# Kernel optimization log

Measured on AMD Instinct MI355X. Metric: run time of the kernel, lower is better.

The kernel has to match this reference:

```python
import jax, jax.numpy as jnp
import numpy as np

# Cost coefficients from MatcherConfig (init_kwargs)
C_CLASS, C_MASK, C_DICE, C_DIST, C_NLL, C_LIK = 2.0, 5.0, 5.0, 1.0, 0.5, 0.5

B, P, Q, E = 8, 16384, 256, 128  # images, pixels (H*W), queries, electrons


def setup_inputs() -> dict:
    key = jax.random.key(0)
    ks = jax.random.split(key, 8)
    mask_mask = jax.random.uniform(ks[0], (B, P, Q)) < 0.10           # sparsity pattern of pred logits
    mask_logit_values = jax.random.normal(ks[1], (B, P, Q), jnp.float32)
    seg_occ = jax.random.uniform(ks[2], (B, P, E)) < 0.05              # sparsity pattern of target segmap
    seg_vals = jax.random.uniform(ks[3], (B, P, E), jnp.float32, 1e-3, 1.0)
    segmap_values = jnp.where(seg_occ, seg_vals, 0.0)
    pred_logits = jax.random.normal(ks[4], (B, Q), jnp.float32)
    pred_positions = jax.random.uniform(ks[5], (B, Q, 2), jnp.float32)
    true_positions = jax.random.uniform(ks[6], (B, E, 2), jnp.float32)
    kd, ko = jax.random.split(ks[7])
    diag = 1.0 + 2.0 * jax.random.uniform(kd, (B, Q, 2), jnp.float32)  # positive diag of scale_tril
    off = 0.3 * jax.random.normal(ko, (B, Q), jnp.float32)
    pred_chol = jnp.zeros((B, Q, 2, 2), jnp.float32)
    pred_chol = pred_chol.at[..., 0, 0].set(diag[..., 0])
    pred_chol = pred_chol.at[..., 1, 1].set(diag[..., 1])
    pred_chol = pred_chol.at[..., 1, 0].set(off)
    image_sizes_xy = jnp.full((B, 2), 128.0, jnp.float32)
    return {
        'pred_logits': pred_logits,
        'mask_logit_values': mask_logit_values,
        'mask_mask': mask_mask,
        'segmap_values': segmap_values,
        'pred_positions': pred_positions,
        'pred_chol': pred_chol,
        'true_positions': true_positions,
        'image_sizes_xy': image_sizes_xy,
    }


def _total_cost(pred_logits, mask_logit_values, segmap_values, pred_positions,
                pred_chol, true_positions, image_sizes_xy, mask_mask):
    sp = jax.nn.softplus
    m = mask_mask
    # --- class cost: BCE(logit, 1) per query -> [B,Q]
    class_cost = sp(-pred_logits)
    # --- mask BCE cost (get_bce_cost): sparse entries only
    pos = jnp.where(m, sp(-mask_logit_values), 0.0)   # BCE vs 1 on nnz entries
    neg = jnp.where(m, sp(mask_logit_values), 0.0)    # BCE vs 0 on nnz entries
    targ = (segmap_values > 0).astype(pos.dtype)      # binarized target segmap
    pos_loss = jnp.einsum('bpq,bpe->bqe', pos, targ)
    neg_loss = neg.sum(1)[:, :, None] - jnp.einsum('bpq,bpe->bqe', neg, targ)
    nnz = jnp.maximum(targ.sum((1, 2)), 1.0)          # target _nnz() per image
    mask_cost = (pos_loss + neg_loss) / nnz[:, None, None]
    # --- dice cost (get_dice_cost): sparse softmax over query dim
    NEG = jnp.asarray(-1e30, mask_logit_values.dtype)
    z = jnp.where(m, mask_logit_values, NEG)
    mx = jnp.max(z, axis=-1, keepdims=True)
    ez = jnp.where(m, jnp.exp(z - mx), 0.0)
    s = ez.sum(-1, keepdims=True)
    pred_p = jnp.where(s > 0, ez / jnp.maximum(s, 1e-30), 0.0)  # [B,P,Q]
    num = 2.0 * jnp.einsum('bpq,bpe->bqe', pred_p, segmap_values)
    den = pred_p.sum(1)[:, :, None] + segmap_values.sum(1)[:, None, :]
    dice_cost = 1.0 - (num + 1.0) / (den + 1.0)
    # --- huber distance cost (delta=1), mean over xy
    d = pred_positions[:, :, None, :] - true_positions[:, None, :, :]  # [B,Q,E,2]
    ad = jnp.abs(d)
    huber_cost = jnp.where(ad < 1.0, 0.5 * d * d, ad - 0.5).mean(-1)
    # --- NLL / likelihood distance costs (MVN with scale_tril)
    mu = pred_positions * image_sizes_xy[:, None, :]
    y = true_positions * image_sizes_xy[:, None, :]
    diff = y[:, None, :, :] - mu[:, :, None, :]        # [B,Q,E,2]
    L00 = pred_chol[..., 0, 0][:, :, None]
    L10 = pred_chol[..., 1, 0][:, :, None]
    L11 = pred_chol[..., 1, 1][:, :, None]
    z0 = diff[..., 0] / L00
    z1 = (diff[..., 1] - L10 * z0) / L11
    nll_cost = 0.5 * (z0 * z0 + z1 * z1) + jnp.log(2.0 * jnp.pi) + jnp.log(L00) + jnp.log(L11)
    lik_cost = 1.0 - jnp.exp(-nll_cost)
    total = (C_CLASS * class_cost[:, :, None] + C_MASK * mask_cost + C_DICE * dice_cost
             + C_DIST * huber_cost + C_NLL * nll_cost + C_LIK * lik_cost)
    return total  # [B, Q, E] stacked per-image cost matrices


def reference(pred_logits, mask_logit_values, mask_mask, segmap_values,
              pred_positions, pred_chol, true_positions, image_sizes_xy):
    return _total_cost(pred_logits, mask_logit_values, segmap_values, pred_positions,
                       pred_chol, true_positions, image_sizes_xy, mask_mask)
```

## Files before the change

kernel.cpp:

```cpp
#include <hip/hip_runtime.h>
#include <cstdint>
#include <cstddef>

typedef float v4f __attribute__((ext_vector_type(4)));
typedef short short8 __attribute__((ext_vector_type(8)));
typedef unsigned short ushort_t;

constexpr int B_ = 8, P_ = 16384, Q_ = 256, E_ = 128;

__device__ __forceinline__ unsigned int f2bf(float f) {
  unsigned int x = __float_as_uint(f);
  x += 0x7FFFu + ((x >> 16) & 1u);
  return x >> 16;
}
__device__ __forceinline__ float softplus_f(float x) {
  return fmaxf(x, 0.f) + __logf(1.f + __expf(-fabsf(x)));
}
__device__ __forceinline__ void gload16(const void* g, void* l) {
  __builtin_amdgcn_global_load_lds((const __attribute__((address_space(1))) void*)g,
                                   (__attribute__((address_space(3))) void*)l,
                                   16, 0, 0);
}

__global__ __launch_bounds__(256, 4) void prep_rows(
    const float* __restrict__ mlv, const int* __restrict__ mask,
    ushort_t* __restrict__ A1T, ushort_t* __restrict__ PPT,
    float* __restrict__ negsum, float* __restrict__ ppsum)
{
  __shared__ unsigned int st[256 * 33];
  const int t = threadIdx.x, w = t >> 6, l = t & 63;
  const int b = blockIdx.x >> 8, cp = blockIdx.x & 255;
  const size_t base = ((size_t)b * P_ + cp * 64) * Q_;
  float accN[4] = {0.f,0.f,0.f,0.f}, accP[4] = {0.f,0.f,0.f,0.f};
  unsigned int a1w[4][4][2], ppw[4][4][2];

#pragma unroll
  for (int g = 0; g < 4; ++g) {
#pragma unroll
    for (int j = 0; j < 4; ++j) { a1w[g][j][0]=0; a1w[g][j][1]=0; ppw[g][j][0]=0; ppw[g][j][1]=0; }
#pragma unroll
    for (int r = 0; r < 4; ++r) {
      const int pl = (w << 4) + (g << 2) + r;
      const float* xp = mlv + base + (size_t)pl * Q_ + l;
      const int*   mp = mask + base + (size_t)pl * Q_ + l;
      float xs[4]; int ms[4];
#pragma unroll
      for (int j = 0; j < 4; ++j) { xs[j] = xp[j * 64]; ms[j] = mp[j * 64]; }
      float ev[4]; float s = 0.f;
#pragma unroll
      for (int j = 0; j < 4; ++j) {
        const bool mm = ms[j] != 0;
        const float xv = xs[j];
        const float e = mm ? __expf(xv) : 0.f;
        ev[j] = e; s += e;
        accN[j] += __logf(1.f + e);
        a1w[g][j][r >> 1] |= f2bf(mm ? -xv : 0.f) << ((r & 1) * 16);
      }
#pragma unroll
      for (int o = 32; o; o >>= 1) s += __shfl_xor(s, o, 64);
      const float inv = (s > 0.f) ? (1.f / s) : 0.f;
#pragma unroll
      for (int j = 0; j < 4; ++j) {
        const float p = ev[j] * inv;
        accP[j] += p;
        ppw[g][j][r >> 1] |= f2bf(p) << ((r & 1) * 16);
      }
    }
  }
  const size_t tb = ((size_t)(b * 256 + cp)) * 16384;
#pragma unroll
  for (int g = 0; g < 4; ++g)
#pragma unroll
    for (int j = 0; j < 4; ++j) {
      const int wb = (l + (j << 6)) * 33 + (w << 3) + (g << 1);
      st[wb] = a1w[g][j][0]; st[wb + 1] = a1w[g][j][1];
    }
  __syncthreads();
  {
    uint4* dst = (uint4*)(A1T + tb);
#pragma unroll
    for (int pass = 0; pass < 8; ++pass) {
      const int gi = pass * 256 + t;
      const int q = gi >> 3, c = (gi & 7) ^ (q & 7);
      const int wd = q * 33 + c * 4;
      uint4 v; v.x = st[wd]; v.y = st[wd+1]; v.z = st[wd+2]; v.w = st[wd+3];
      dst[gi] = v;
    }
  }
  __syncthreads();
#pragma unroll
  for (int g = 0; g < 4; ++g)
#pragma unroll
    for (int j = 0; j < 4; ++j) {
      const int wb = (l + (j << 6)) * 33 + (w << 3) + (g << 1);
      st[wb] = ppw[g][j][0]; st[wb + 1] = ppw[g][j][1];
    }
  __syncthreads();
  {
    uint4* dst = (uint4*)(PPT + tb);
#pragma unroll
    for (int pass = 0; pass < 8; ++pass) {
      const int gi = pass * 256 + t;
      const int q = gi >> 3, c = (gi & 7) ^ (q & 7);
      const int wd = q * 33 + c * 4;
      uint4 v; v.x = st[wd]; v.y = st[wd+1]; v.z = st[wd+2]; v.w = st[wd+3];
      dst[gi] = v;
    }
  }
  __syncthreads();
  float* red = (float*)st;
#pragma unroll
  for (int j = 0; j < 4; ++j) red[w * 256 + l + (j << 6)] = accN[j];
  __syncthreads();
  {
    const float sn = red[t] + red[256 + t] + red[512 + t] + red[768 + t];
    atomicAdd(&negsum[b * 256 + t], sn);
  }
  __syncthreads();
#pragma unroll
  for (int j = 0; j < 4; ++j) red[w * 256 + l + (j << 6)] = accP[j];
  __syncthreads();
  {
    const float sq = red[t] + red[256 + t] + red[512 + t] + red[768 + t];
    atomicAdd(&ppsum[b * 256 + t], sq);
  }
}

__global__ __launch_bounds__(256, 4) void prep_seg(
    const float* __restrict__ seg, ushort_t* __restrict__ SGT, ushort_t* __restrict__ SGB,
    float* __restrict__ segsum, float* __restrict__ nnzb)
{
  __shared__ unsigned int st[128 * 33];
  const int t = threadIdx.x, w = t >> 6, l = t & 63;
  const int b = blockIdx.x >> 8, cp = blockIdx.x & 255;
  const size_t base = ((size_t)b * P_ + cp * 64) * E_;
  float accS[2] = {0.f, 0.f}; float cnt = 0.f;
  unsigned int sgw[4][2][2], sbw[4][2][2];
#pragma unroll
  for (int g = 0; g < 4; ++g) {
#pragma unroll
    for (int j = 0; j < 2; ++j) { sgw[g][j][0]=0; sgw[g][j][1]=0; sbw[g][j][0]=0; sbw[g][j][1]=0; }
#pragma unroll
    for (int r = 0; r < 4; ++r) {
      const int pl = (w << 4) + (g << 2) + r;
      const float* vp = seg + base + (size_t)pl * E_ + l;
#pragma unroll
      for (int j = 0; j < 2; ++j) {
        const float v = vp[j * 64];
        const bool nz = v > 0.f;
        accS[j] += v; cnt += nz ? 1.f : 0.f;
        sgw[g][j][r >> 1] |= f2bf(v) << ((r & 1) * 16);
        sbw[g][j][r >> 1] |= (nz ? 0x3F80u : 0u) << ((r & 1) * 16);
      }
    }
  }
  const size_t tb = ((size_t)(b * 256 + cp)) * 8192;
#pragma unroll
  for (int g = 0; g < 4; ++g)
#pragma unroll
    for (int j = 0; j < 2; ++j) {
      const int wb = (l + (j << 6)) * 33 + (w << 3) + (g << 1);
      st[wb] = sgw[g][j][0]; st[wb + 1] = sgw[g][j][1];
    }
  __syncthreads();
  {
    uint4* dst = (uint4*)(SGT + tb);
#pragma unroll
    for (int pass = 0; pass < 4; ++pass) {
      const int gi = pass * 256 + t;
      const int q = gi >> 3, c = (gi & 7) ^ (q & 7);
      const int wd = q * 33 + c * 4;
      uint4 v; v.x = st[wd]; v.y = st[wd+1]; v.z = st[wd+2]; v.w = st[wd+3];
      dst[gi] = v;
    }
  }
  __syncthreads();
#pragma unroll
  for (int g = 0; g < 4; ++g)
#pragma unroll
    for (int j = 0; j < 2; ++j) {
      const int wb = (l + (j << 6)) * 33 + (w << 3) + (g << 1);
      st[wb] = sbw[g][j][0]; st[wb + 1] = sbw[g][j][1];
    }
  __syncthreads();
  {
    uint4* dst = (uint4*)(SGB + tb);
#pragma unroll
    for (int pass = 0; pass < 4; ++pass) {
      const int gi = pass * 256 + t;
      const int q = gi >> 3, c = (gi & 7) ^ (q & 7);
      const int wd = q * 33 + c * 4;
      uint4 v; v.x = st[wd]; v.y = st[wd+1]; v.z = st[wd+2]; v.w = st[wd+3];
      dst[gi] = v;
    }
  }
  __syncthreads();
  float* red = (float*)st;
#pragma unroll
  for (int j = 0; j < 2; ++j) red[w * 128 + l + (j << 6)] = accS[j];
  __syncthreads();
  if (t < 128) {
    const float ss = red[t] + red[128 + t] + red[256 + t] + red[384 + t];
    atomicAdd(&segsum[b * 128 + t], ss);
  }
#pragma unroll
  for (int o = 32; o; o >>= 1) cnt += __shfl_xor(cnt, o, 64);
  if (l == 0) atomicAdd(&nnzb[b], cnt);
}

__global__ __launch_bounds__(256, 2) void gemm_mfma(
    const ushort_t* __restrict__ A1T, const ushort_t* __restrict__ PPT,
    const ushort_t* __restrict__ SGT, const ushort_t* __restrict__ SGB,
    float* __restrict__ part)
{
  __shared__ __align__(16) char lds[32768];
  const int id = blockIdx.x;
  const int ks = id & 15, qt = (id >> 4) & 1, g = (id >> 5) & 1, b = id >> 6;
  const ushort_t* Aall = g ? PPT : A1T;
  const ushort_t* Ball = g ? SGT : SGB;
  const int t = threadIdx.x, l = t & 63, w = t >> 6;
  const int lm = l & 15, quad = l >> 4;
  const int wm = w & 1, wn = w >> 1;
  v4f acc[4][4];
#pragma unroll
  for (int i = 0; i < 4; ++i)
#pragma unroll
    for (int j = 0; j < 4; ++j) acc[i][j] = (v4f)0.f;
  const size_t cp0 = (size_t)b * 256 + ks * 16;
  const char* gA = (const char*)(Aall + cp0 * 16384 + qt * 8192);
  const char* gB = (const char*)(Ball + cp0 * 8192);
  const int off = t * 16;

  for (int it = 0; it < 16; ++it) {
    __syncthreads();
    const char* pa = gA + (size_t)it * 32768;
    const char* pb = gB + (size_t)it * 16384;
    gload16(pa + off,          lds + off);
    gload16(pa + off + 4096,   lds + off + 4096);
    gload16(pa + off + 8192,   lds + off + 8192);
    gload16(pa + off + 12288,  lds + off + 12288);
    gload16(pb + off,          lds + 16384 + off);
    gload16(pb + off + 4096,   lds + 16384 + off + 4096);
    gload16(pb + off + 8192,   lds + 16384 + off + 8192);
    gload16(pb + off + 12288,  lds + 16384 + off + 12288);
    __syncthreads();
#pragma unroll
    for (int k32 = 0; k32 < 2; ++k32) {
      short8 af[4], bf[4];
      const int ach = ((k32 << 2) | quad) ^ (lm & 7);
#pragma unroll
      for (int i = 0; i < 4; ++i) {
        af[i] = *(const short8*)(lds + (wm * 64 + i * 16 + lm) * 128 + ach * 16);
        bf[i] = *(const short8*)(lds + 16384 + (wn * 64 + i * 16 + lm) * 128 + ach * 16);
      }
#pragma unroll
      for (int i = 0; i < 4; ++i)
#pragma unroll
        for (int j = 0; j < 4; ++j)
          acc[i][j] = __builtin_amdgcn_mfma_f32_16x16x32_bf16(af[i], bf[j], acc[i][j], 0, 0, 0);
    }
  }
  float* pout = part + (size_t)(g * 8 + b) * 32768;
#pragma unroll
  for (int i = 0; i < 4; ++i)
#pragma unroll
    for (int r = 0; r < 4; ++r) {
      const int q = qt * 128 + wm * 64 + i * 16 + quad * 4 + r;
#pragma unroll
      for (int j = 0; j < 4; ++j) {
        const int e = wn * 64 + j * 16 + lm;
        atomicAdd(&pout[q * 128 + e], acc[i][j][r]);
      }
    }
}

__global__ __launch_bounds__(128) void epilogue(
    const float* __restrict__ part,
    const float* __restrict__ negsum, const float* __restrict__ ppsum,
    const float* __restrict__ segsum, const float* __restrict__ nnzb,
    const float* __restrict__ logits, const float* __restrict__ ppos,
    const float* __restrict__ chol, const float* __restrict__ tpos,
    const float* __restrict__ imgsz, float* __restrict__ out)
{
  const int bq = blockIdx.x;
  const int b = bq >> 8;
  const int e = threadIdx.x;
  const int qe = (bq & 255) * 128 + e;
  const float g1 = part[(size_t)b * 32768 + qe];
  const float g2 = part[(size_t)(8 + b) * 32768 + qe];

  const float nnz = fmaxf(nnzb[b], 1.f);
  const float mask_cost = (negsum[bq] + g1) / nnz;
  const float dice = 1.f - (2.f * g2 + 1.f) / (ppsum[bq] + segsum[b * 128 + e] + 1.f);
  const float cls = softplus_f(-logits[bq]);
  const float px = ppos[bq * 2], py = ppos[bq * 2 + 1];
  const float tx = tpos[(b * 128 + e) * 2], ty = tpos[(b * 128 + e) * 2 + 1];
  const float dx = px - tx, dy = py - ty;
  const float ax = fabsf(dx), ay = fabsf(dy);
  const float hx = (ax < 1.f) ? 0.5f * dx * dx : ax - 0.5f;
  const float hy = (ay < 1.f) ? 0.5f * dy * dy : ay - 0.5f;
  const float huber = 0.5f * (hx + hy);
  const float sx = imgsz[b * 2], sy = imgsz[b * 2 + 1];
  const float L00 = chol[bq * 4 + 0], L10 = chol[bq * 4 + 2], L11 = chol[bq * 4 + 3];
  const float d0 = (tx - px) * sx, d1 = (ty - py) * sy;
  const float z0 = d0 / L00;
  const float z1 = (d1 - L10 * z0) / L11;
  const float nll = 0.5f * (z0 * z0 + z1 * z1) + 1.8378770664093453f + __logf(L00) + __logf(L11);
  const float lik = 1.f - __expf(-nll);
  out[bq * 128 + e] = 2.f * cls + 5.f * mask_cost + 5.f * dice + huber + 0.5f * nll + 0.5f * lik;
}

extern "C" void kernel_launch(void* const* d_in, const int* in_sizes, int n_in,
                              void* d_out, int out_size, void* d_ws, size_t ws_size,
                              hipStream_t stream)
{
  (void)in_sizes; (void)n_in; (void)out_size; (void)ws_size;
  const float* logits = (const float*)d_in[0];
  const float* mlv    = (const float*)d_in[1];
  const int*   mask   = (const int*)d_in[2];
  const float* seg    = (const float*)d_in[3];
  const float* ppos   = (const float*)d_in[4];
  const float* chol   = (const float*)d_in[5];
  const float* tpos   = (const float*)d_in[6];
  const float* imgsz  = (const float*)d_in[7];

  char* ws = (char*)d_ws;
  ushort_t* A1T = (ushort_t*)(ws);
  ushort_t* PPT = (ushort_t*)(ws + 67108864);
  ushort_t* SGT = (ushort_t*)(ws + 134217728);
  ushort_t* SGB = (ushort_t*)(ws + 167772160);
  float* part   = (float*)(ws + 201326592);
  float* negsum = (float*)(ws + 203423744);
  float* ppsum  = (float*)(ws + 203431936);
  float* segsum = (float*)(ws + 203440128);
  float* nnzb   = (float*)(ws + 203444224);

  hipMemsetAsync(ws + 201326592, 0, 2117696, stream);
  prep_seg<<<2048, 256, 0, stream>>>(seg, SGT, SGB, segsum, nnzb);
  prep_rows<<<2048, 256, 0, stream>>>(mlv, mask, A1T, PPT, negsum, ppsum);
  gemm_mfma<<<512, 256, 0, stream>>>(A1T, PPT, SGT, SGB, part);
  epilogue<<<2048, 128, 0, stream>>>(part, negsum, ppsum, segsum, nnzb,
                                     logits, ppos, chol, tpos, imgsz, (float*)d_out);
}
```

Before: 512.6 us.

## Vectorize prep kernel loads with float4, prefetching, and a new LDS transpose layout

Both preprocessing kernels now have each lane read four consecutive columns with 16-byte loads and prefetch the next row pair. They pack bf16 pairs of adjacent rows in registers and write them to LDS in a row-major padded layout, then read it back transposed. prep_seg builds the binary mask tile from the bf16 value tile during the store, so it needs one LDS staging pass instead of two. The goal is fewer, wider global load instructions and less LDS traffic in these memory-bound kernels. The cost is more register pressure and strided LDS reads, which may cause bank conflicts.

Result: slower. 523.4 us (+2.1%).

```diff
diff --git a/kernel.cpp b/kernel.cpp
--- a/kernel.cpp
+++ b/kernel.cpp
@@ -27,181 +27,168 @@
     ushort_t* __restrict__ A1T, ushort_t* __restrict__ PPT,
     float* __restrict__ negsum, float* __restrict__ ppsum)
 {
-  __shared__ unsigned int st[256 * 33];
+  __shared__ unsigned int st[32 * 260];
   const int t = threadIdx.x, w = t >> 6, l = t & 63;
   const int b = blockIdx.x >> 8, cp = blockIdx.x & 255;
-  const size_t base = ((size_t)b * P_ + cp * 64) * Q_;
+  const size_t base = ((size_t)b * P_ + (size_t)cp * 64) * Q_;
+  const float* rbase = mlv + base + (size_t)(w * 16) * Q_ + 4 * l;
+  const int*   mbase = mask + base + (size_t)(w * 16) * Q_ + 4 * l;
   float accN[4] = {0.f,0.f,0.f,0.f}, accP[4] = {0.f,0.f,0.f,0.f};
-  unsigned int a1w[4][4][2], ppw[4][4][2];
-
-#pragma unroll
-  for (int g = 0; g < 4; ++g) {
-#pragma unroll
-    for (int j = 0; j < 4; ++j) { a1w[g][j][0]=0; a1w[g][j][1]=0; ppw[g][j][0]=0; ppw[g][j][1]=0; }
-#pragma unroll
-    for (int r = 0; r < 4; ++r) {
-      const int pl = (w << 4) + (g << 2) + r;
-      const float* xp = mlv + base + (size_t)pl * Q_ + l;
-      const int*   mp = mask + base + (size_t)pl * Q_ + l;
-      float xs[4]; int ms[4];
-#pragma unroll
-      for (int j = 0; j < 4; ++j) { xs[j] = xp[j * 64]; ms[j] = mp[j * 64]; }
-      float ev[4]; float s = 0.f;
-#pragma unroll
-      for (int j = 0; j < 4; ++j) {
-        const bool mm = ms[j] != 0;
-        const float xv = xs[j];
-        const float e = mm ? __expf(xv) : 0.f;
-        ev[j] = e; s += e;
-        accN[j] += __logf(1.f + e);
-        a1w[g][j][r >> 1] |= f2bf(mm ? -xv : 0.f) << ((r & 1) * 16);
-      }
-#pragma unroll
-      for (int o = 32; o; o >>= 1) s += __shfl_xor(s, o, 64);
-      const float inv = (s > 0.f) ? (1.f / s) : 0.f;
-#pragma unroll
-      for (int j = 0; j < 4; ++j) {
-        const float p = ev[j] * inv;
-        accP[j] += p;
-        ppw[g][j][r >> 1] |= f2bf(p) << ((r & 1) * 16);
-      }
-    }
+  uint4 ppw[8];
+
+  float4 X0 = *(const float4*)(rbase);
+  float4 X1 = *(const float4*)(rbase + Q_);
+  int4   M0 = *(const int4*)(mbase);
+  int4   M1 = *(const int4*)(mbase + Q_);
+#pragma unroll
+  for (int m = 0; m < 8; ++m) {
+    const int nm = (m < 7) ? m + 1 : 7;
+    float4 nX0 = *(const float4*)(rbase + (2 * nm) * Q_);
+    float4 nX1 = *(const float4*)(rbase + (2 * nm + 1) * Q_);
+    int4   nM0 = *(const int4*)(mbase + (2 * nm) * Q_);
+    int4   nM1 = *(const int4*)(mbase + (2 * nm + 1) * Q_);
+    const float xs0[4] = {X0.x, X0.y, X0.z, X0.w};
+    const float xs1[4] = {X1.x, X1.y, X1.z, X1.w};
+    const int   ms0[4] = {M0.x, M0.y, M0.z, M0.w};
+    const int   ms1[4] = {M1.x, M1.y, M1.z, M1.w};
+    float e0[4], e1[4]; float s0 = 0.f, s1 = 0.f;
+    unsigned int a1w[4];
+#pragma unroll
+    for (int j = 0; j < 4; ++j) {
+      const bool q0 = ms0[j] != 0, q1 = ms1[j] != 0;
+      const float ev0 = q0 ? __expf(xs0[j]) : 0.f;
+      const float ev1 = q1 ? __expf(xs1[j]) : 0.f;
+      e0[j] = ev0; e1[j] = ev1; s0 += ev0; s1 += ev1;
+      accN[j] += __logf(1.f + ev0) + __logf(1.f + ev1);
+      a1w[j] = f2bf(q0 ? -xs0[j] : 0.f) | (f2bf(q1 ? -xs1[j] : 0.f) << 16);
+    }
+#pragma unroll
+    for (int o = 32; o; o >>= 1) { s0 += __shfl_xor(s0, o, 64); s1 += __shfl_xor(s1, o, 64); }
+    const float i0 = (s0 > 0.f) ? (1.f / s0) : 0.f;
+    const float i1 = (s1 > 0.f) ? (1.f / s1) : 0.f;
+    unsigned int pw[4];
+#pragma unroll
+    for (int j = 0; j < 4; ++j) {
+      const float p0 = e0[j] * i0, p1 = e1[j] * i1;
+      accP[j] += p0 + p1;
+      pw[j] = f2bf(p0) | (f2bf(p1) << 16);
+    }
+    ppw[m].x = pw[0]; ppw[m].y = pw[1]; ppw[m].z = pw[2]; ppw[m].w = pw[3];
+    uint4 av; av.x = a1w[0]; av.y = a1w[1]; av.z = a1w[2]; av.w = a1w[3];
+    *(uint4*)(st + (w * 8 + m) * 260 + 4 * l) = av;
+    X0 = nX0; X1 = nX1; M0 = nM0; M1 = nM1;
   }
   const size_t tb = ((size_t)(b * 256 + cp)) * 16384;
-#pragma unroll
-  for (int g = 0; g < 4; ++g)
-#pragma unroll
-    for (int j = 0; j < 4; ++j) {
-      const int wb = (l + (j << 6)) * 33 + (w << 3) + (g << 1);
-      st[wb] = a1w[g][j][0]; st[wb + 1] = a1w[g][j][1];
-    }
   __syncthreads();
   {
     uint4* dst = (uint4*)(A1T + tb);
 #pragma unroll
     for (int pass = 0; pass < 8; ++pass) {
       const int gi = pass * 256 + t;
-      const int q = gi >> 3, c = (gi & 7) ^ (q & 7);
-      const int wd = q * 33 + c * 4;
-      uint4 v; v.x = st[wd]; v.y = st[wd+1]; v.z = st[wd+2]; v.w = st[wd+3];
+      const int q = gi >> 3, cc = (gi & 7) ^ (q & 7);
+      const int wb = cc * 1040 + q;
+      uint4 v; v.x = st[wb]; v.y = st[wb + 260]; v.z = st[wb + 520]; v.w = st[wb + 780];
       dst[gi] = v;
     }
   }
   __syncthreads();
 #pragma unroll
-  for (int g = 0; g < 4; ++g)
-#pragma unroll
-    for (int j = 0; j < 4; ++j) {
-      const int wb = (l + (j << 6)) * 33 + (w << 3) + (g << 1);
-      st[wb] = ppw[g][j][0]; st[wb + 1] = ppw[g][j][1];
-    }
+  for (int m = 0; m < 8; ++m) *(uint4*)(st + (w * 8 + m) * 260 + 4 * l) = ppw[m];
   __syncthreads();
   {
     uint4* dst = (uint4*)(PPT + tb);
 #pragma unroll
     for (int pass = 0; pass < 8; ++pass) {
       const int gi = pass * 256 + t;
-      const int q = gi >> 3, c = (gi & 7) ^ (q & 7);
-      const int wd = q * 33 + c * 4;
-      uint4 v; v.x = st[wd]; v.y = st[wd+1]; v.z = st[wd+2]; v.w = st[wd+3];
+      const int q = gi >> 3, cc = (gi & 7) ^ (q & 7);
+      const int wb = cc * 1040 + q;
+      uint4 v; v.x = st[wb]; v.y = st[wb + 260]; v.z = st[wb + 520]; v.w = st[wb + 780];
       dst[gi] = v;
     }
   }
   __syncthreads();
   float* red = (float*)st;
 #pragma unroll
-  for (int j = 0; j < 4; ++j) red[w * 256 + l + (j << 6)] = accN[j];
-  __syncthreads();
-  {
-    const float sn = red[t] + red[256 + t] + red[512 + t] + red[768 + t];
-    atomicAdd(&negsum[b * 256 + t], sn);
-  }
-  __syncthreads();
-#pragma unroll
-  for (int j = 0; j < 4; ++j) red[w * 256 + l + (j << 6)] = accP[j];
-  __syncthreads();
-  {
-    const float sq = red[t] + red[256 + t] + red[512 + t] + red[768 + t];
-    atomicAdd(&ppsum[b * 256 + t], sq);
-  }
+  for (int j = 0; j < 4; ++j) red[w * 256 + 4 * l + j] = accN[j];
+  __syncthreads();
+  { const float sn = red[t] + red[256 + t] + red[512 + t] + red[768 + t];
+    atomicAdd(&negsum[b * 256 + t], sn); }
+  __syncthreads();
+#pragma unroll
+  for (int j = 0; j < 4; ++j) red[w * 256 + 4 * l + j] = accP[j];
+  __syncthreads();
+  { const float sq = red[t] + red[256 + t] + red[512 + t] + red[768 + t];
+    atomicAdd(&ppsum[b * 256 + t], sq); }
 }
 
 __global__ __launch_bounds__(256, 4) void prep_seg(
     const float* __restrict__ seg, ushort_t* __restrict__ SGT, ushort_t* __restrict__ SGB,
     float* __restrict__ segsum, float* __restrict__ nnzb)
 {
-  __shared__ unsigned int st[128 * 33];
+  __shared__ unsigned int st[32 * 132];
   const int t = threadIdx.x, w = t >> 6, l = t & 63;
+  const int side = l >> 5, e0 = (l & 31) * 4;
   const int b = blockIdx.x >> 8, cp = blockIdx.x & 255;
-  const size_t base = ((size_t)b * P_ + cp * 64) * E_;
-  float accS[2] = {0.f, 0.f}; float cnt = 0.f;
-  unsigned int sgw[4][2][2], sbw[4][2][2];
-#pragma unroll
-  for (int g = 0; g < 4; ++g) {
-#pragma unroll
-    for (int j = 0; j < 2; ++j) { sgw[g][j][0]=0; sgw[g][j][1]=0; sbw[g][j][0]=0; sbw[g][j][1]=0; }
-#pragma unroll
-    for (int r = 0; r < 4; ++r) {
-      const int pl = (w << 4) + (g << 2) + r;
-      const float* vp = seg + base + (size_t)pl * E_ + l;
-#pragma unroll
-      for (int j = 0; j < 2; ++j) {
-        const float v = vp[j * 64];
-        const bool nz = v > 0.f;
-        accS[j] += v; cnt += nz ? 1.f : 0.f;
-        sgw[g][j][r >> 1] |= f2bf(v) << ((r & 1) * 16);
-        sbw[g][j][r >> 1] |= (nz ? 0x3F80u : 0u) << ((r & 1) * 16);
-      }
-    }
+  const size_t base = ((size_t)b * P_ + (size_t)cp * 64) * E_;
+  const float* rb = seg + base + (size_t)(w * 16 + side) * E_ + e0;
+  float accS[4] = {0.f,0.f,0.f,0.f}; float cnt = 0.f;
+
+  float4 V = *(const float4*)(rb);
+#pragma unroll
+  for (int m = 0; m < 8; ++m) {
+    const int nm = (m < 7) ? m + 1 : 7;
+    float4 nV = *(const float4*)(rb + (2 * nm) * E_);
+    const float vs[4] = {V.x, V.y, V.z, V.w};
+    uint2 own;
+    own.x = f2bf(vs[0]) | (f2bf(vs[1]) << 16);
+    own.y = f2bf(vs[2]) | (f2bf(vs[3]) << 16);
+#pragma unroll
+    for (int j = 0; j < 4; ++j) { accS[j] += vs[j]; cnt += (vs[j] > 0.f) ? 1.f : 0.f; }
+    uint2 part;
+    part.x = (unsigned)__shfl_xor((int)own.x, 32, 64);
+    part.y = (unsigned)__shfl_xor((int)own.y, 32, 64);
+    unsigned int wa, wb2;
+    if (side == 0) {
+      wa  = (own.x & 0xFFFFu) | (part.x << 16);
+      wb2 = (own.x >> 16) | (part.x & 0xFFFF0000u);
+    } else {
+      wa  = (part.y & 0xFFFFu) | (own.y << 16);
+      wb2 = (part.y >> 16) | (own.y & 0xFFFF0000u);
+    }
+    uint2 wv; wv.x = wa; wv.y = wb2;
+    *(uint2*)(st + (w * 8 + m) * 132 + e0 + side * 2) = wv;
+    V = nV;
   }
   const size_t tb = ((size_t)(b * 256 + cp)) * 8192;
-#pragma unroll
-  for (int g = 0; g < 4; ++g)
-#pragma unroll
-    for (int j = 0; j < 2; ++j) {
-      const int wb = (l + (j << 6)) * 33 + (w << 3) + (g << 1);
-      st[wb] = sgw[g][j][0]; st[wb + 1] = sgw[g][j][1];
-    }
   __syncthreads();
   {
-    uint4* dst = (uint4*)(SGT + tb);
+    uint4* dT = (uint4*)(SGT + tb);
+    uint4* dB = (uint4*)(SGB + tb);
 #pragma unroll
     for (int pass = 0; pass < 4; ++pass) {
       const int gi = pass * 256 + t;
-      const int q = gi >> 3, c = (gi & 7) ^ (q & 7);
-      const int wd = q * 33 + c * 4;
-      uint4 v; v.x = st[wd]; v.y = st[wd+1]; v.z = st[wd+2]; v.w = st[wd+3];
-      dst[gi] = v;
-    }
-  }
-  __syncthreads();
-#pragma unroll
-  for (int g = 0; g < 4; ++g)
-#pragma unroll
-    for (int j = 0; j < 2; ++j) {
-      const int wb = (l + (j << 6)) * 33 + (w << 3) + (g << 1);
-      st[wb] = sbw[g][j][0]; st[wb + 1] = sbw[g][j][1];
-    }
-  __syncthreads();
-  {
-    uint4* dst = (uint4*)(SGB + tb);
-#pragma unroll
-    for (int pass = 0; pass < 4; ++pass) {
-      const int gi = pass * 256 + t;
-      const int q = gi >> 3, c = (gi & 7) ^ (q & 7);
-      const int wd = q * 33 + c * 4;
-      uint4 v; v.x = st[wd]; v.y = st[wd+1]; v.z = st[wd+2]; v.w = st[wd+3];
-      dst[gi] = v;
+      const int e = gi >> 3, cc = (gi & 7) ^ (e & 7);
+      const int wb = cc * 528 + e;
+      uint4 v; v.x = st[wb]; v.y = st[wb + 132]; v.z = st[wb + 264]; v.w = st[wb + 396];
+      dT[gi] = v;
+      uint4 bv;
+      bv.x = ((v.x & 0xFFFFu) ? 0x3F80u : 0u) | ((v.x >> 16) ? 0x3F800000u : 0u);
+      bv.y = ((v.y & 0xFFFFu) ? 0x3F80u : 0u) | ((v.y >> 16) ? 0x3F800000u : 0u);
+      bv.z = ((v.z & 0xFFFFu) ? 0x3F80u : 0u) | ((v.z >> 16) ? 0x3F800000u : 0u);
+      bv.w = ((v.w & 0xFFFFu) ? 0x3F80u : 0u) | ((v.w >> 16) ? 0x3F800000u : 0u);
+      dB[gi] = bv;
     }
   }
   __syncthreads();
   float* red = (float*)st;
 #pragma unroll
-  for (int j = 0; j < 2; ++j) red[w * 128 + l + (j << 6)] = accS[j];
+  for (int j = 0; j < 4; ++j) red[(w * 2 + side) * 128 + e0 + j] = accS[j];
   __syncthreads();
   if (t < 128) {
-    const float ss = red[t] + red[128 + t] + red[256 + t] + red[384 + t];
-    atomicAdd(&segsum[b * 128 + t], ss);
+    float s = 0.f;
+#pragma unroll
+    for (int k = 0; k < 8; ++k) s += red[k * 128 + t];
+    atomicAdd(&segsum[b * 128 + t], s);
   }
 #pragma unroll
   for (int o = 32; o; o >>= 1) cnt += __shfl_xor(cnt, o, 64);
```
